# Performance work log

Hardware: AMD Instinct MI355X
Metric: run time of the kernel (lower is better)

## Reference

```python
import jax, jax.numpy as jnp
import numpy as np

N_NODES = 25000
N_EDGES = 400000
N_GRAPHS = 1000
HID = 185
IN_CH = 9
EPS = 1e-5  # BatchNorm eps (eval mode: uses running stats)


def setup_inputs() -> dict:
    key = jax.random.key(0)
    ks = jax.random.split(key, 12)
    x = jax.random.normal(ks[0], (N_NODES, IN_CH), jnp.float32)
    edge_index = jax.random.randint(ks[1], (2, N_EDGES), 0, N_NODES, jnp.int32)
    batch = jnp.sort(jax.random.randint(ks[2], (N_NODES,), 0, N_GRAPHS, jnp.int32))
    W0 = jax.random.normal(ks[3], (IN_CH, HID), jnp.float32) * 0.3
    b0 = jnp.zeros((HID,), jnp.float32)
    W_h = jax.random.normal(ks[4], (3, HID, HID), jnp.float32) * 0.07
    b_h = jnp.zeros((3, HID), jnp.float32)
    bn_gamma = 1.0 + 0.1 * jax.random.normal(ks[5], (4, HID), jnp.float32)
    bn_beta = 0.1 * jax.random.normal(ks[6], (4, HID), jnp.float32)
    bn_mean = 0.1 * jax.random.normal(ks[7], (4, HID), jnp.float32)
    bn_var = jax.random.uniform(ks[8], (4, HID), jnp.float32, 0.5, 1.5)
    W_jk = jax.random.normal(ks[9], (4 * HID, HID), jnp.float32) * 0.05
    b_jk = jnp.zeros((HID,), jnp.float32)
    W_out = jax.random.normal(ks[10], (HID, 1), jnp.float32) * 0.1
    b_out = jnp.zeros((1,), jnp.float32)
    return dict(x=x, edge_index=edge_index, batch=batch, W0=W0, b0=b0,
                W_h=W_h, b_h=b_h, bn_gamma=bn_gamma, bn_beta=bn_beta,
                bn_mean=bn_mean, bn_var=bn_var, W_jk=W_jk, b_jk=b_jk,
                W_out=W_out, b_out=b_out)


def reference(x, edge_index, batch, W0, b0, W_h, b_h, bn_gamma, bn_beta,
              bn_mean, bn_var, W_jk, b_jk, W_out, b_out):
    N = x.shape[0]
    # GCN normalization with self-loops (gcn_norm, edge_weight = 1)
    loop = jnp.arange(N, dtype=edge_index.dtype)
    src = jnp.concatenate([edge_index[0], loop])  # [E+N]
    dst = jnp.concatenate([edge_index[1], loop])  # [E+N]
    deg = jax.ops.segment_sum(jnp.ones_like(dst, dtype=x.dtype), dst, num_segments=N)
    dis = jnp.where(deg > 0, jax.lax.rsqrt(jnp.maximum(deg, 1.0)), 0.0)
    enorm = dis[src] * dis[dst]  # [E+N]

    def gcn_conv(h, W, b):
        h = h @ W                                   # [N, HID]
        msg = h[src] * enorm[:, None]               # gather + scale, [E+N, HID]
        return jax.ops.segment_sum(msg, dst, num_segments=N) + b

    def bn_relu(h, i):
        h = (h - bn_mean[i]) * jax.lax.rsqrt(bn_var[i] + EPS) * bn_gamma[i] + bn_beta[i]
        return jax.nn.relu(h)  # dropout is identity in eval mode

    xs = []
    h = bn_relu(gcn_conv(x, W0, b0), 0)
    xs.append(h)
    for i in range(3):
        h = bn_relu(gcn_conv(h, W_h[i], b_h[i]), i + 1)
        xs.append(h)
    # JumpingKnowledge 'cat' + internal lin (740 -> 185)
    h = jnp.concatenate(xs, axis=-1) @ W_jk + b_jk  # [N, HID]
    # global_max_pool over graphs
    pooled = jax.ops.segment_max(h, batch, num_segments=N_GRAPHS)  # [G, HID]
    return pooled @ W_out + b_out  # [G, 1]
```

## Files before the change

kernel.cpp:

```cpp
#include <hip/hip_runtime.h>
#include <hip/hip_bf16.h>

#define N_NODES 25000
#define N_EDGES 400000
#define N_GRAPHS 1000
#define HID 185
#define EPS 1e-5f
#define XPITCH 768

typedef __attribute__((ext_vector_type(8))) short bf16x8;
typedef __attribute__((ext_vector_type(4))) float f32x4;

__device__ __forceinline__ short f2bf(float f) {
    union { float f; unsigned u; } v; v.f = f;
    unsigned r = v.u + 0x7FFFu + ((v.u >> 16) & 1u);
    return (short)(r >> 16);
}
__device__ __forceinline__ float bfl(unsigned u) { return __uint_as_float(u << 16); }
__device__ __forceinline__ float bfh(unsigned u) { return __uint_as_float(u & 0xFFFF0000u); }
__device__ __forceinline__ unsigned pk2(float lo, float hi) {
    return (unsigned)(unsigned short)f2bf(lo) | ((unsigned)(unsigned short)f2bf(hi) << 16);
}

#define HW (3 * 192 * 192)
#define JW (192 * 768)
#define CNTPAD 25024
__global__ void k_setup(const float* __restrict__ W_h, const float* __restrict__ W_jk,
                        const float* __restrict__ b0, const float* __restrict__ b_h,
                        const float* __restrict__ gamma, const float* __restrict__ beta,
                        const float* __restrict__ mean, const float* __restrict__ var,
                        int* __restrict__ cnt,
                        short* __restrict__ Wt_h, short* __restrict__ Wt_jk,
                        float* __restrict__ bnsc, float* __restrict__ bnsh) {
    int idx = blockIdx.x * 256 + threadIdx.x;
    if (idx < CNTPAD) { cnt[idx] = 0; return; }
    int p = idx - CNTPAD;
    if (p < HW) {
        int l = p / (192 * 192);
        int r = p % (192 * 192);
        int n = r / 192, k = r % 192;
        float v = (n < HID && k < HID) ? W_h[(l * HID + k) * HID + n] : 0.0f;
        Wt_h[p] = f2bf(v);
    } else if (p < HW + JW) {
        int j2 = p - HW;
        int n = j2 / 768, kk = j2 % 768;
        int l = kk / 192, j = kk % 192;
        float v = (n < HID && j < HID) ? W_jk[(l * HID + j) * HID + n] : 0.0f;
        Wt_jk[j2] = f2bf(v);
    } else if (p < HW + JW + 4 * 192) {
        int li = p - HW - JW;
        int l = li / 192, c = li % 192;
        float sc = 0.0f, sh = 0.0f;
        if (c < HID) {
            float bb = (l == 0) ? b0[c] : b_h[(l - 1) * HID + c];
            sc = rsqrtf(var[l * HID + c] + EPS) * gamma[l * HID + c];
            sh = (bb - mean[l * HID + c]) * sc + beta[l * HID + c];
        }
        bnsc[li] = sc;
        bnsh[li] = sh;
    }
}

__global__ void k_deg(const int* __restrict__ dst, int* cnt, int E) {
    int i = blockIdx.x * blockDim.x + threadIdx.x;
    if (i < E) atomicAdd(&cnt[dst[i]], 1);
}

__global__ __launch_bounds__(256) void k_scan_part(const int* __restrict__ cnt,
                                                   int* __restrict__ bsum,
                                                   float* __restrict__ dis, int N) {
    int i = blockIdx.x * 256 + threadIdx.x;
    int v = (i < N) ? cnt[i] : 0;
    if (i < N) dis[i] = rsqrtf((float)(v + 1));
    #pragma unroll
    for (int off = 32; off; off >>= 1) v += __shfl_down(v, off);
    __shared__ int s[4];
    if ((threadIdx.x & 63) == 0) s[threadIdx.x >> 6] = v;
    __syncthreads();
    if (threadIdx.x == 0) bsum[blockIdx.x] = s[0] + s[1] + s[2] + s[3];
}

__global__ __launch_bounds__(256) void k_scan_add(const int* __restrict__ cnt,
                                                  const int* __restrict__ bsum,
                                                  int* __restrict__ rowptr, int N) {
    __shared__ int s[256];
    const int t = threadIdx.x;
    const int b = blockIdx.x;
    int partial = 0;
    for (int i = t; i < b; i += 256) partial += bsum[i];
    s[t] = partial; __syncthreads();
    for (int off = 128; off; off >>= 1) {
        if (t < off) s[t] += s[t + off];
        __syncthreads();
    }
    const int base = s[0];
    __syncthreads();
    int i = b * 256 + t;
    int v = (i < N) ? cnt[i] : 0;
    s[t] = v; __syncthreads();
    for (int off = 1; off < 256; off <<= 1) {
        int x2 = (t >= off) ? s[t - off] : 0;
        __syncthreads();
        s[t] += x2;
        __syncthreads();
    }
    if (i < N) rowptr[i] = base + s[t] - v;
}

__global__ void k_scatter(const int* __restrict__ src, const int* __restrict__ dst,
                          const float* __restrict__ dis,
                          int* rowptr, int* __restrict__ csr_src,
                          float* __restrict__ csr_w, int E) {
    int e = blockIdx.x * blockDim.x + threadIdx.x;
    if (e < E) {
        int d = dst[e];
        int s = src[e];
        int o = atomicAdd(&rowptr[d], 1);
        csr_src[o] = s;
        csr_w[o] = dis[s];
    }
}

__global__ __launch_bounds__(192) void k_gemm0f(const float* __restrict__ x,
                                                const float* __restrict__ dis,
                                                const int* __restrict__ rowptr,
                                                const int* __restrict__ csr_src,
                                                const float* __restrict__ csr_w,
                                                const float* __restrict__ W,
                                                const float* __restrict__ bnsc,
                                                const float* __restrict__ bnsh,
                                                short* __restrict__ xcat, int N) {
    __shared__ float As[72];
    const int tid = threadIdx.x;
    const int r0 = blockIdx.x * 8;
    if (tid < 72) {
        int r = tid & 7, k = tid >> 3;
        int row = r0 + r;
        float val = 0.0f;
        if (row < N && k < 9) {
            float dn = dis[row];
            float acc = x[row * 9 + k] * dn;
            int end = rowptr[row];
            int e = row ? rowptr[row - 1] : 0;
            for (; e + 4 <= end; e += 4) {
                int s0 = csr_src[e], s1 = csr_src[e+1], s2 = csr_src[e+2], s3 = csr_src[e+3];
                float w0 = csr_w[e], w1 = csr_w[e+1], w2 = csr_w[e+2], w3 = csr_w[e+3];
                acc += x[s0*9+k]*w0 + x[s1*9+k]*w1 + x[s2*9+k]*w2 + x[s3*9+k]*w3;
            }
            for (; e < end; ++e)
                acc += x[csr_src[e] * 9 + k] * csr_w[e];
            val = acc * dn;
        }
        As[tid] = val;
    }
    __syncthreads();
    const int c = tid;
    float res[8];
    #pragma unroll
    for (int r = 0; r < 8; ++r) res[r] = 0.0f;
    if (c < HID) {
        float acc[8] = {0,0,0,0,0,0,0,0};
        for (int k = 0; k < 9; ++k) {
            float w = W[k * HID + c];
            #pragma unroll
            for (int r = 0; r < 8; ++r) acc[r] += As[k * 8 + r] * w;
        }
        float sc = bnsc[c], sh = bnsh[c];
        #pragma unroll
        for (int r = 0; r < 8; ++r)
            res[r] = fmaxf(acc[r] * sc + sh, 0.0f);
    }
    #pragma unroll
    for (int r = 0; r < 8; ++r) {
        int row = r0 + r;
        if (row < N) xcat[row * XPITCH + c] = (c < HID) ? f2bf(res[r]) : (short)0;
    }
}

template<int KCH>
__global__ __launch_bounds__(256) void k_mgemm(const short* __restrict__ A,
                                               const short* __restrict__ Bt,
                                               short* __restrict__ Cout, int N) {
    const int tid = threadIdx.x;
    const int wave = tid >> 6;
    const int lane = tid & 63;
    const int quad = lane >> 4;
    const int lm = lane & 15;
    const int r0 = blockIdx.x * 64;
    const int KTOT = KCH * 32;
    const short* Ab = A + (size_t)(r0 + lm) * XPITCH + quad * 8;
    const short* Bb = Bt + (size_t)(wave * 48 + lm) * KTOT + quad * 8;

    f32x4 acc[4][3];
    #pragma unroll
    for (int i = 0; i < 4; ++i)
        #pragma unroll
        for (int j = 0; j < 3; ++j) acc[i][j] = (f32x4){0.f, 0.f, 0.f, 0.f};

    for (int g = 0; g < KCH / 6; ++g) {
        #pragma unroll
        for (int j = 0; j < 6; ++j) {
            const int kc = g * 6 + j;
            bf16x8 b[3];
            #pragma unroll
            for (int nt = 0; nt < 3; ++nt)
                b[nt] = *(const bf16x8*)(Bb + (size_t)nt * 16 * KTOT + kc * 32);
            #pragma unroll
            for (int mt = 0; mt < 4; ++mt) {
                bf16x8 a = *(const bf16x8*)(Ab + (size_t)mt * 16 * XPITCH + kc * 32);
                #pragma unroll
                for (int nt = 0; nt < 3; ++nt)
                    acc[mt][nt] = __builtin_amdgcn_mfma_f32_16x16x32_bf16(
                        a, b[nt], acc[mt][nt], 0, 0, 0);
            }
        }
    }
    #pragma unroll
    for (int mt = 0; mt < 4; ++mt) {
        #pragma unroll
        for (int nt = 0; nt < 3; ++nt) {
            int col = wave * 48 + nt * 16 + lm;
            #pragma unroll
            for (int r = 0; r < 4; ++r) {
                int row = r0 + mt * 16 + quad * 4 + r;
                if (row < N) Cout[row * 192 + col] = f2bf(acc[mt][nt][r]);
            }
        }
    }
}

__global__ __launch_bounds__(256) void k_aggr_bn(const short* __restrict__ tmp16,
                                                 const float* __restrict__ dis,
                                                 const int* __restrict__ rowptr,
                                                 const int* __restrict__ csr_src,
                                                 const float* __restrict__ csr_w,
                                                 const float* __restrict__ bnsc,
                                                 const float* __restrict__ bnsh,
                                                 short* __restrict__ outp, int N) {
    int n = (blockIdx.x << 2) + (threadIdx.x >> 6);
    if (n >= N) return;
    int lane = threadIdx.x & 63;
    int c0 = (lane < 48) ? (lane << 2) : 0;
    float dn = dis[n];
    float a0, a1, a2, a3;
    {
        uint2 v = *(const uint2*)(tmp16 + (size_t)n * 192 + c0);
        a0 = bfl(v.x) * dn; a1 = bfh(v.x) * dn; a2 = bfl(v.y) * dn; a3 = bfh(v.y) * dn;
    }
    int end = rowptr[n];
    int e = n ? rowptr[n - 1] : 0;
    for (; e + 4 <= end; e += 4) {
        int s0 = csr_src[e], s1 = csr_src[e + 1], s2 = csr_src[e + 2], s3 = csr_src[e + 3];
        float w0 = csr_w[e], w1 = csr_w[e + 1], w2 = csr_w[e + 2], w3 = csr_w[e + 3];
        uint2 v0 = *(const uint2*)(tmp16 + (size_t)s0 * 192 + c0);
        uint2 v1 = *(const uint2*)(tmp16 + (size_t)s1 * 192 + c0);
        uint2 v2 = *(const uint2*)(tmp16 + (size_t)s2 * 192 + c0);
        uint2 v3 = *(const uint2*)(tmp16 + (size_t)s3 * 192 + c0);
        a0 += bfl(v0.x) * w0; a1 += bfh(v0.x) * w0; a2 += bfl(v0.y) * w0; a3 += bfh(v0.y) * w0;
        a0 += bfl(v1.x) * w1; a1 += bfh(v1.x) * w1; a2 += bfl(v1.y) * w1; a3 += bfh(v1.y) * w1;
        a0 += bfl(v2.x) * w2; a1 += bfh(v2.x) * w2; a2 += bfl(v2.y) * w2; a3 += bfh(v2.y) * w2;
        a0 += bfl(v3.x) * w3; a1 += bfh(v3.x) * w3; a2 += bfl(v3.y) * w3; a3 += bfh(v3.y) * w3;
    }
    for (; e < end; ++e) {
        int s = csr_src[e];
        float w = csr_w[e];
        uint2 v = *(const uint2*)(tmp16 + (size_t)s * 192 + c0);
        a0 += bfl(v.x) * w; a1 += bfh(v.x) * w; a2 += bfl(v.y) * w; a3 += bfh(v.y) * w;
    }
    float4 sc = *(const float4*)(bnsc + c0);
    float4 sh = *(const float4*)(bnsh + c0);
    float o0 = fmaxf(a0 * dn * sc.x + sh.x, 0.0f);
    float o1 = fmaxf(a1 * dn * sc.y + sh.y, 0.0f);
    float o2 = fmaxf(a2 * dn * sc.z + sh.z, 0.0f);
    float o3 = fmaxf(a3 * dn * sc.w + sh.w, 0.0f);
    if (lane < 48) {
        uint2 p;
        p.x = pk2(o0, o1);
        p.y = pk2(o2, o3);
        *(uint2*)(outp + (size_t)n * XPITCH + c0) = p;
    }
}

__global__ __launch_bounds__(192) void k_pool_out(const short* __restrict__ jk,
                                                  const int* __restrict__ batch,
                                                  const float* __restrict__ b_jk,
                                                  const float* __restrict__ W_out,
                                                  const float* __restrict__ b_out,
                                                  float* __restrict__ out, int N) {
    __shared__ int bounds[2];
    __shared__ float partial[3];
    const int g = blockIdx.x;
    const int tid = threadIdx.x;
    if (tid < 2) {
        int key = g + tid;
        int lo = 0, hi = N;
        while (lo < hi) {
            int mid = (lo + hi) >> 1;
            if (batch[mid] < key) lo = mid + 1; else hi = mid;
        }
        bounds[tid] = lo;
    }
    __syncthreads();
    const int beg = bounds[0], end = bounds[1];
    float mx = -3.4e38f;
    for (int n = beg; n < end; ++n)
        mx = fmaxf(mx, bfl((unsigned)(unsigned short)jk[(size_t)n * 192 + tid]));
    float p = (tid < HID) ? (mx + b_jk[tid]) * W_out[tid] : 0.0f;
    #pragma unroll
    for (int off = 32; off; off >>= 1) p += __shfl_down(p, off);
    if ((tid & 63) == 0) partial[tid >> 6] = p;
    __syncthreads();
    if (tid == 0) out[g] = partial[0] + partial[1] + partial[2] + b_out[0];
}

extern "C" void kernel_launch(void* const* d_in, const int* in_sizes, int n_in,
                              void* d_out, int out_size, void* d_ws, size_t ws_size,
                              hipStream_t stream) {
    const float* x      = (const float*)d_in[0];
    const int*   ei     = (const int*)  d_in[1];
    const int*   batch  = (const int*)  d_in[2];
    const float* W0     = (const float*)d_in[3];
    const float* b0     = (const float*)d_in[4];
    const float* W_h    = (const float*)d_in[5];
    const float* b_h    = (const float*)d_in[6];
    const float* gamma  = (const float*)d_in[7];
    const float* beta   = (const float*)d_in[8];
    const float* mean   = (const float*)d_in[9];
    const float* var    = (const float*)d_in[10];
    const float* W_jk   = (const float*)d_in[11];
    const float* b_jk   = (const float*)d_in[12];
    const float* W_out  = (const float*)d_in[13];
    const float* b_out  = (const float*)d_in[14];
    float* out = (float*)d_out;

    const int N = N_NODES, E = N_EDGES, G = N_GRAPHS;
    const int NB = (N + 255) / 256;

    float* dis   = (float*)d_ws;
    float* csr_w = dis + 25024;
    float* bnsc  = csr_w + 400000;
    float* bnsh  = bnsc + 768;
    short* xcat  = (short*)(bnsh + 768);
    short* tmp16 = xcat + 19200000;
    short* Wt_h  = tmp16 + 4800000;
    short* Wt_jk = Wt_h + 110592;
    int* rowptr  = (int*)(Wt_jk + 147456);
    int* cnt     = rowptr + 25024;
    int* csr_src = cnt + 25024;
    int* bsum    = csr_src + 400000;

    const int* src = ei;
    const int* dst = ei + E;

    k_setup<<<(CNTPAD + HW + JW + 4 * 192 + 255) / 256, 256, 0, stream>>>(
        W_h, W_jk, b0, b_h, gamma, beta, mean, var, cnt, Wt_h, Wt_jk, bnsc, bnsh);
    k_deg<<<(E + 255) / 256, 256, 0, stream>>>(dst, cnt, E);
    k_scan_part<<<NB, 256, 0, stream>>>(cnt, bsum, dis, N);
    k_scan_add<<<NB, 256, 0, stream>>>(cnt, bsum, rowptr, N);
    k_scatter<<<(E + 255) / 256, 256, 0, stream>>>(src, dst, dis, rowptr, csr_src, csr_w, E);

    k_gemm0f<<<(N + 7) / 8, 192, 0, stream>>>(x, dis, rowptr, csr_src, csr_w,
                                              W0, bnsc, bnsh, xcat, N);

    const int MB = (N + 63) / 64;
    for (int l = 1; l < 4; ++l) {
        k_mgemm<6><<<MB, 256, 0, stream>>>(xcat + (l - 1) * 192,
                                           Wt_h + (l - 1) * 192 * 192, tmp16, N);
        k_aggr_bn<<<(N + 3) / 4, 256, 0, stream>>>(tmp16, dis, rowptr, csr_src, csr_w,
                                                   bnsc + l * 192, bnsh + l * 192,
                                                   xcat + l * 192, N);
    }

    k_mgemm<24><<<MB, 256, 0, stream>>>(xcat, Wt_jk, tmp16, N);

    k_pool_out<<<G, 192, 0, stream>>>(tmp16, batch, b_jk, W_out, b_out, out, N);
}
```

Baseline: 339.0 us.

## Pack CSR edges as int2, split layer-0 aggregation, stage GEMM tiles in LDS

The CSR source index and edge weight are interleaved into one int2 array, so each edge needs one load instead of two in the aggregation kernels. The first-layer fused aggregate-plus-GEMM is split into a dense per-node aggregation kernel and a separate small GEMM, which spreads the gather across more threads. The MFMA GEMM now stages A and B tiles through padded shared memory with barriers per K-chunk instead of loading fragments straight from global memory. The changes add an extra launch and an intermediate buffer, and the LDS staging adds two barriers per K step with no double buffering.

New measurement: 305.4 us. 9.9% less time.

```diff
diff --git a/kernel.cpp b/kernel.cpp
--- a/kernel.cpp
+++ b/kernel.cpp
@@ -7,6 +7,7 @@
 #define HID 185
 #define EPS 1e-5f
 #define XPITCH 768
+#define APITCH 36
 
 typedef __attribute__((ext_vector_type(8))) short bf16x8;
 typedef __attribute__((ext_vector_type(4))) float f32x4;
@@ -109,49 +110,53 @@
 
 __global__ void k_scatter(const int* __restrict__ src, const int* __restrict__ dst,
                           const float* __restrict__ dis,
-                          int* rowptr, int* __restrict__ csr_src,
-                          float* __restrict__ csr_w, int E) {
+                          int* rowptr, int2* __restrict__ csr, int E) {
     int e = blockIdx.x * blockDim.x + threadIdx.x;
     if (e < E) {
         int d = dst[e];
         int s = src[e];
         int o = atomicAdd(&rowptr[d], 1);
-        csr_src[o] = s;
-        csr_w[o] = dis[s];
-    }
-}
-
-__global__ __launch_bounds__(192) void k_gemm0f(const float* __restrict__ x,
-                                                const float* __restrict__ dis,
-                                                const int* __restrict__ rowptr,
-                                                const int* __restrict__ csr_src,
-                                                const float* __restrict__ csr_w,
-                                                const float* __restrict__ W,
-                                                const float* __restrict__ bnsc,
-                                                const float* __restrict__ bnsh,
-                                                short* __restrict__ xcat, int N) {
-    __shared__ float As[72];
+        csr[o] = make_int2(s, __float_as_int(dis[s]));
+    }
+}
+
+__global__ void k_aggr0(const float* __restrict__ x, const float* __restrict__ dis,
+                        const int* __restrict__ rowptr, const int2* __restrict__ csr,
+                        float* __restrict__ xa, int N) {
+    int idx = blockIdx.x * blockDim.x + threadIdx.x;
+    int n = idx >> 4;
+    int c = idx & 15;
+    if (n >= N || c >= 9) return;
+    float dn = dis[n];
+    float acc = x[n * 9 + c] * dn;
+    int end = rowptr[n];
+    int e = n ? rowptr[n - 1] : 0;
+    for (; e + 4 <= end; e += 4) {
+        int2 p0 = csr[e], p1 = csr[e + 1], p2 = csr[e + 2], p3 = csr[e + 3];
+        acc += x[p0.x * 9 + c] * __int_as_float(p0.y)
+             + x[p1.x * 9 + c] * __int_as_float(p1.y)
+             + x[p2.x * 9 + c] * __int_as_float(p2.y)
+             + x[p3.x * 9 + c] * __int_as_float(p3.y);
+    }
+    for (; e < end; ++e) {
+        int2 p = csr[e];
+        acc += x[p.x * 9 + c] * __int_as_float(p.y);
+    }
+    xa[n * 9 + c] = acc * dn;
+}
+
+__global__ __launch_bounds__(192) void k_gemm0(const float* __restrict__ A,
+                                               const float* __restrict__ W,
+                                               const float* __restrict__ bnsc,
+                                               const float* __restrict__ bnsh,
+                                               short* __restrict__ xcat, int N) {
+    __shared__ float As[8 * 9];
     const int tid = threadIdx.x;
     const int r0 = blockIdx.x * 8;
-    if (tid < 72) {
-        int r = tid & 7, k = tid >> 3;
+    for (int idx = tid; idx < 72; idx += 192) {
+        int r = idx & 7, k = idx >> 3;
         int row = r0 + r;
-        float val = 0.0f;
-        if (row < N && k < 9) {
-            float dn = dis[row];
-            float acc = x[row * 9 + k] * dn;
-            int end = rowptr[row];
-            int e = row ? rowptr[row - 1] : 0;
-            for (; e + 4 <= end; e += 4) {
-                int s0 = csr_src[e], s1 = csr_src[e+1], s2 = csr_src[e+2], s3 = csr_src[e+3];
-                float w0 = csr_w[e], w1 = csr_w[e+1], w2 = csr_w[e+2], w3 = csr_w[e+3];
-                acc += x[s0*9+k]*w0 + x[s1*9+k]*w1 + x[s2*9+k]*w2 + x[s3*9+k]*w3;
-            }
-            for (; e < end; ++e)
-                acc += x[csr_src[e] * 9 + k] * csr_w[e];
-            val = acc * dn;
-        }
-        As[tid] = val;
+        As[idx] = (row < N) ? A[row * 9 + k] : 0.0f;
     }
     __syncthreads();
     const int c = tid;
@@ -181,6 +186,8 @@
 __global__ __launch_bounds__(256) void k_mgemm(const short* __restrict__ A,
                                                const short* __restrict__ Bt,
                                                short* __restrict__ Cout, int N) {
+    __shared__ short As[64 * APITCH];
+    __shared__ short Bs[192 * APITCH];
     const int tid = threadIdx.x;
     const int wave = tid >> 6;
     const int lane = tid & 63;
@@ -188,8 +195,7 @@
     const int lm = lane & 15;
     const int r0 = blockIdx.x * 64;
     const int KTOT = KCH * 32;
-    const short* Ab = A + (size_t)(r0 + lm) * XPITCH + quad * 8;
-    const short* Bb = Bt + (size_t)(wave * 48 + lm) * KTOT + quad * 8;
+    const int arow = tid >> 2, aseg = tid & 3;
 
     f32x4 acc[4][3];
     #pragma unroll
@@ -197,23 +203,35 @@
         #pragma unroll
         for (int j = 0; j < 3; ++j) acc[i][j] = (f32x4){0.f, 0.f, 0.f, 0.f};
 
-    for (int g = 0; g < KCH / 6; ++g) {
-        #pragma unroll
-        for (int j = 0; j < 6; ++j) {
-            const int kc = g * 6 + j;
-            bf16x8 b[3];
+    for (int kc = 0; kc < KCH; ++kc) {
+        const int k0 = kc * 32;
+        {
+            int grow = r0 + arow;
+            bf16x8 v = (bf16x8){0,0,0,0,0,0,0,0};
+            if (grow < N) v = *(const bf16x8*)(A + grow * XPITCH + k0 + aseg * 8);
+            *(bf16x8*)(As + arow * APITCH + aseg * 8) = v;
+        }
+        #pragma unroll
+        for (int i = 0; i < 3; ++i) {
+            int u = tid + i * 256;
+            int n = u >> 2, seg = u & 3;
+            bf16x8 v = *(const bf16x8*)(Bt + n * KTOT + k0 + seg * 8);
+            *(bf16x8*)(Bs + n * APITCH + seg * 8) = v;
+        }
+        __syncthreads();
+        bf16x8 a[4], b[3];
+        #pragma unroll
+        for (int mt = 0; mt < 4; ++mt)
+            a[mt] = *(const bf16x8*)(As + (mt * 16 + lm) * APITCH + quad * 8);
+        #pragma unroll
+        for (int nt = 0; nt < 3; ++nt)
+            b[nt] = *(const bf16x8*)(Bs + (wave * 48 + nt * 16 + lm) * APITCH + quad * 8);
+        #pragma unroll
+        for (int mt = 0; mt < 4; ++mt)
             #pragma unroll
             for (int nt = 0; nt < 3; ++nt)
-                b[nt] = *(const bf16x8*)(Bb + (size_t)nt * 16 * KTOT + kc * 32);
-            #pragma unroll
-            for (int mt = 0; mt < 4; ++mt) {
-                bf16x8 a = *(const bf16x8*)(Ab + (size_t)mt * 16 * XPITCH + kc * 32);
-                #pragma unroll
-                for (int nt = 0; nt < 3; ++nt)
-                    acc[mt][nt] = __builtin_amdgcn_mfma_f32_16x16x32_bf16(
-                        a, b[nt], acc[mt][nt], 0, 0, 0);
-            }
-        }
+                acc[mt][nt] = __builtin_amdgcn_mfma_f32_16x16x32_bf16(a[mt], b[nt], acc[mt][nt], 0, 0, 0);
+        __syncthreads();
     }
     #pragma unroll
     for (int mt = 0; mt < 4; ++mt) {
@@ -232,8 +250,7 @@
 __global__ __launch_bounds__(256) void k_aggr_bn(const short* __restrict__ tmp16,
                                                  const float* __restrict__ dis,
                                                  const int* __restrict__ rowptr,
-                                                 const int* __restrict__ csr_src,
-                                                 const float* __restrict__ csr_w,
+                                                 const int2* __restrict__ csr,
                                                  const float* __restrict__ bnsc,
                                                  const float* __restrict__ bnsh,
                                                  short* __restrict__ outp, int N) {
@@ -250,21 +267,22 @@
     int end = rowptr[n];
     int e = n ? rowptr[n - 1] : 0;
     for (; e + 4 <= end; e += 4) {
-        int s0 = csr_src[e], s1 = csr_src[e + 1], s2 = csr_src[e + 2], s3 = csr_src[e + 3];
-        float w0 = csr_w[e], w1 = csr_w[e + 1], w2 = csr_w[e + 2], w3 = csr_w[e + 3];
-        uint2 v0 = *(const uint2*)(tmp16 + (size_t)s0 * 192 + c0);
-        uint2 v1 = *(const uint2*)(tmp16 + (size_t)s1 * 192 + c0);
-        uint2 v2 = *(const uint2*)(tmp16 + (size_t)s2 * 192 + c0);
-        uint2 v3 = *(const uint2*)(tmp16 + (size_t)s3 * 192 + c0);
+        int2 p0 = csr[e], p1 = csr[e + 1], p2 = csr[e + 2], p3 = csr[e + 3];
+        float w0 = __int_as_float(p0.y), w1 = __int_as_float(p1.y);
+        float w2 = __int_as_float(p2.y), w3 = __int_as_float(p3.y);
+        uint2 v0 = *(const uint2*)(tmp16 + (size_t)p0.x * 192 + c0);
+        uint2 v1 = *(const uint2*)(tmp16 + (size_t)p1.x * 192 + c0);
+        uint2 v2 = *(const uint2*)(tmp16 + (size_t)p2.x * 192 + c0);
+        uint2 v3 = *(const uint2*)(tmp16 + (size_t)p3.x * 192 + c0);
         a0 += bfl(v0.x) * w0; a1 += bfh(v0.x) * w0; a2 += bfl(v0.y) * w0; a3 += bfh(v0.y) * w0;
         a0 += bfl(v1.x) * w1; a1 += bfh(v1.x) * w1; a2 += bfl(v1.y) * w1; a3 += bfh(v1.y) * w1;
         a0 += bfl(v2.x) * w2; a1 += bfh(v2.x) * w2; a2 += bfl(v2.y) * w2; a3 += bfh(v2.y) * w2;
         a0 += bfl(v3.x) * w3; a1 += bfh(v3.x) * w3; a2 += bfl(v3.y) * w3; a3 += bfh(v3.y) * w3;
     }
     for (; e < end; ++e) {
-        int s = csr_src[e];
-        float w = csr_w[e];
-        uint2 v = *(const uint2*)(tmp16 + (size_t)s * 192 + c0);
+        int2 p = csr[e];
+        float w = __int_as_float(p.y);
+        uint2 v = *(const uint2*)(tmp16 + (size_t)p.x * 192 + c0);
         a0 += bfl(v.x) * w; a1 += bfh(v.x) * w; a2 += bfl(v.y) * w; a3 += bfh(v.y) * w;
     }
     float4 sc = *(const float4*)(bnsc + c0);
@@ -337,17 +355,17 @@
     const int NB = (N + 255) / 256;
 
     float* dis   = (float*)d_ws;
-    float* csr_w = dis + 25024;
-    float* bnsc  = csr_w + 400000;
+    float* xa    = dis + 25024;
+    float* bnsc  = xa + 225024;
     float* bnsh  = bnsc + 768;
-    short* xcat  = (short*)(bnsh + 768);
+    int2*  csr   = (int2*)(bnsh + 768);
+    short* xcat  = (short*)(csr + 400000);
     short* tmp16 = xcat + 19200000;
     short* Wt_h  = tmp16 + 4800000;
     short* Wt_jk = Wt_h + 110592;
     int* rowptr  = (int*)(Wt_jk + 147456);
     int* cnt     = rowptr + 25024;
-    int* csr_src = cnt + 25024;
-    int* bsum    = csr_src + 400000;
+    int* bsum    = cnt + 25024;
 
     const int* src = ei;
     const int* dst = ei + E;
@@ -357,16 +375,16 @@
     k_deg<<<(E + 255) / 256, 256, 0, stream>>>(dst, cnt, E);
     k_scan_part<<<NB, 256, 0, stream>>>(cnt, bsum, dis, N);
     k_scan_add<<<NB, 256, 0, stream>>>(cnt, bsum, rowptr, N);
-    k_scatter<<<(E + 255) / 256, 256, 0, stream>>>(src, dst, dis, rowptr, csr_src, csr_w, E);
-
-    k_gemm0f<<<(N + 7) / 8, 192, 0, stream>>>(x, dis, rowptr, csr_src, csr_w,
-                                              W0, bnsc, bnsh, xcat, N);
+    k_scatter<<<(E + 255) / 256, 256, 0, stream>>>(src, dst, dis, rowptr, csr, E);
+
+    k_aggr0<<<(N * 16 + 255) / 256, 256, 0, stream>>>(x, dis, rowptr, csr, xa, N);
+    k_gemm0<<<(N + 7) / 8, 192, 0, stream>>>(xa, W0, bnsc, bnsh, xcat, N);
 
     const int MB = (N + 63) / 64;
     for (int l = 1; l < 4; ++l) {
         k_mgemm<6><<<MB, 256, 0, stream>>>(xcat + (l - 1) * 192,
                                            Wt_h + (l - 1) * 192 * 192, tmp16, N);
-        k_aggr_bn<<<(N + 3) / 4, 256, 0, stream>>>(tmp16, dis, rowptr, csr_src, csr_w,
+        k_aggr_bn<<<(N + 3) / 4, 256, 0, stream>>>(tmp16, dis, rowptr, csr,
                                                    bnsc + l * 192, bnsh + l * 192,
                                                    xcat + l * 192, N);
     }
```
